# Kernel optimization log

Hardware: AMD Instinct MI355X
Metric: run time of the kernel (lower is better)

The kernel has to match this reference:

```python
import jax, jax.numpy as jnp
import numpy as np

DC_WZ = 15
ETA = 0.1
RADIUS = DC_WZ // 2  # 7
EPS = 1e-3


def avg_pool2d(x, k, pad):
    # torch F.avg_pool2d default: zero padding, count_include_pad=True -> divide by k*k always
    s = jax.lax.reduce_window(
        x, 0.0, jax.lax.add,
        window_dimensions=(1, 1, k, k),
        window_strides=(1, 1, 1, 1),
        padding=[(0, 0), (0, 0), (pad, pad), (pad, pad)])
    return s / float(k * k)


def min_pool2d_replicate(x, k, pad):
    # replicate (edge) pad then VALID min-pool, matching -max_pool2d(-pad(x, replicate))
    xp = jnp.pad(x, ((0, 0), (0, 0), (pad, pad), (pad, pad)), mode='edge')
    return jax.lax.reduce_window(
        xp, jnp.inf, jax.lax.min,
        window_dimensions=(1, 1, k, k),
        window_strides=(1, 1, 1, 1),
        padding='VALID')


def guided_filter(guide, src, radius, eps=EPS):
    k = 2 * radius + 1
    mean_I = avg_pool2d(guide, k, radius)
    mean_p = avg_pool2d(src, k, radius)
    mean_Ip = avg_pool2d(guide * src, k, radius)
    cov_Ip = mean_Ip - mean_I * mean_p
    mean_II = avg_pool2d(guide * guide, k, radius)
    var_I = mean_II - mean_I * mean_I
    a = cov_Ip / (var_I + eps)
    b = mean_p - a * mean_I
    mean_a = avg_pool2d(a, k, radius)
    mean_b = avg_pool2d(b, k, radius)
    return mean_a * guide + mean_b


def setup_inputs() -> dict:
    key = jax.random.key(0)
    k1, k2 = jax.random.split(key)
    smoky_image = jax.random.uniform(k1, (16, 3, 512, 512), dtype=jnp.float32)
    rho_DNN = jax.random.uniform(k2, (16, 3, 512, 512), dtype=jnp.float32)
    return {"smoky_image": smoky_image, "rho_DNN": rho_DNN}


def reference(smoky_image, rho_DNN):
    # dark channel: per-pixel min over RGB, then 15x15 min-pool with replicate pad
    dc_pixel = jnp.min(smoky_image, axis=-3, keepdims=True)  # [B,1,H,W]
    dc_coarse = min_pool2d_replicate(dc_pixel, DC_WZ, RADIUS)
    guide_I = jnp.mean(smoky_image, axis=-3, keepdims=True)
    dc_refined = guided_filter(guide_I, dc_coarse, RADIUS, EPS)
    dc_refined = jax.lax.stop_gradient(dc_refined)  # torch: no_grad + detach
    dc_rho = (ETA + dc_refined) / (ETA + 1.0) * (1.0 - rho_DNN)
    return smoky_image - dc_rho
```

## Files before the change

kernel.cpp:

```cpp
#include <hip/hip_runtime.h>

#define BATCH 16
#define HH 512
#define WW 512
#define PLANE (HH*WW)

#define LDS_WAIT()   asm volatile("s_waitcnt lgkmcnt(0)" ::: "memory")
#define WAVE_FENCE() asm volatile("" ::: "memory")

#define T1 64
#define HALO 7
#define LW (T1 + 2*HALO)

__global__ __launch_bounds__(256) void k1_guide_minpool(
    const float* __restrict__ smoky, float* __restrict__ guide, float* __restrict__ p)
{
    __shared__ float dcp[LW*LW];
    __shared__ float vmn[T1*LW];
    int nwg = gridDim.x;
    int wg = (blockIdx.x & 7) * (nwg >> 3) + (blockIdx.x >> 3);
    int img  = wg >> 6;
    int tile = wg & 63;
    int y0 = (tile >> 3) * T1;
    int x0 = (tile & 7) * T1;
    int t = threadIdx.x;
    const float* s0 = smoky + (size_t)img * 3 * PLANE;
    float* gpl = guide + (size_t)img * PLANE;
    float* ppl = p     + (size_t)img * PLANE;

    for (int i = t; i < LW*LW; i += 256) {
        int ly = i / LW, lx = i - ly * LW;
        int iy = y0 - HALO + ly, ix = x0 - HALO + lx;
        int cy = min(max(iy, 0), HH-1);
        int cx = min(max(ix, 0), WW-1);
        const float* bp = s0 + cy * WW + cx;
        float c0 = bp[0], c1 = bp[PLANE], c2 = bp[2*PLANE];
        dcp[i] = fminf(fminf(c0, c1), c2);
        if (ly >= HALO && ly < HALO+T1 && lx >= HALO && lx < HALO+T1)
            gpl[iy * WW + ix] = (c0 + c1 + c2) * (1.0f/3.0f);
    }
    __syncthreads();
    for (int i = t; i < T1*LW; i += 256) {
        int r = i / LW, c = i - r * LW;
        float m = dcp[r*LW + c];
        #pragma unroll
        for (int d = 1; d < 15; ++d) m = fminf(m, dcp[(r+d)*LW + c]);
        vmn[i] = m;
    }
    __syncthreads();
    for (int i = t; i < T1*T1; i += 256) {
        int r = i >> 6, c = i & 63;
        float m = vmn[r*LW + c];
        #pragma unroll
        for (int d = 1; d < 15; ++d) m = fminf(m, vmn[r*LW + c + d]);
        ppl[(y0+r)*WW + x0 + c] = m;
    }
}

#define RS2 16

__global__ __launch_bounds__(256) void k2_ab(
    const float* __restrict__ guide, const float* __restrict__ p,
    float* __restrict__ aO, float* __restrict__ bO)
{
    __shared__ float ls[4][4][80];
    int nwg = gridDim.x;
    int wg = (blockIdx.x & 7) * (nwg >> 3) + (blockIdx.x >> 3);
    int w = threadIdx.x >> 6, l = threadIdx.x & 63;
    int gw = wg * 4 + w;
    int img   = gw >> 8;
    int cg    = (gw >> 5) & 7;
    int strip = gw & 31;
    int y0 = strip * RS2;
    int c0 = cg * 64;
    const float* gP = guide + (size_t)img * PLANE;
    const float* pP = p     + (size_t)img * PLANE;
    float* aPl = aO + (size_t)img * PLANE;
    float* bPl = bO + (size_t)img * PLANE;

    int col0 = c0 - 7 + l;
    int col1 = c0 + 57 + l;
    bool v0 = (col0 >= 0);
    bool v1 = (l < 14) && (col1 < WW);

    float sI0=0,sII0=0,sP0=0,sIp0=0;
    float sI1=0,sII1=0,sP1=0,sIp1=0;

    auto loadrow = [&](int y, float& I0, float& Q0, float& I1, float& Q1) {
        I0 = 0.f; Q0 = 0.f; I1 = 0.f; Q1 = 0.f;
        if ((unsigned)y < (unsigned)HH) {
            const float* gr = gP + (size_t)y * WW;
            const float* pr = pP + (size_t)y * WW;
            if (v0) { I0 = gr[col0]; Q0 = pr[col0]; }
            if (v1) { I1 = gr[col1]; Q1 = pr[col1]; }
        }
    };

    for (int r = y0 - 8; r <= y0 + 6; ++r) {
        float I0,Q0,I1,Q1; loadrow(r, I0,Q0,I1,Q1);
        sI0+=I0; sII0+=I0*I0; sP0+=Q0; sIp0+=I0*Q0;
        sI1+=I1; sII1+=I1*I1; sP1+=Q1; sIp1+=I1*Q1;
    }
    float aI0,aQ0,aI1,aQ1, bI0,bQ0,bI1,bQ1;
    loadrow(y0 + 7, aI0,aQ0,aI1,aQ1);
    loadrow(y0 - 8, bI0,bQ0,bI1,bQ1);

    float* L = &ls[w][0][0];
    const float inv225 = 1.0f/225.0f;
    for (int y = y0; y < y0 + RS2; ++y) {
        sI0 += aI0 - bI0;  sII0 += aI0*aI0 - bI0*bI0;
        sP0 += aQ0 - bQ0;  sIp0 += aI0*aQ0 - bI0*bQ0;
        sI1 += aI1 - bI1;  sII1 += aI1*aI1 - bI1*bI1;
        sP1 += aQ1 - bQ1;  sIp1 += aI1*aQ1 - bI1*bQ1;
        loadrow(y + 8, aI0,aQ0,aI1,aQ1);
        loadrow(y - 7, bI0,bQ0,bI1,bQ1);
        L[l] = sI0; L[80+l] = sII0; L[160+l] = sP0; L[240+l] = sIp0;
        if (l < 14) { L[64+l] = sI1; L[144+l] = sII1; L[224+l] = sP1; L[304+l] = sIp1; }
        LDS_WAIT();
        float SI=0,SII=0,SP=0,SIp=0;
        #pragma unroll
        for (int d = 0; d < 15; ++d) {
            SI  += L[l+d];
            SII += L[80+l+d];
            SP  += L[160+l+d];
            SIp += L[240+l+d];
        }
        WAVE_FENCE();
        float mI = SI*inv225, mP = SP*inv225;
        float va = (SIp*inv225 - mI*mP) / (SII*inv225 - mI*mI + 1e-3f);
        size_t off = (size_t)y*WW + c0 + l;
        aPl[off] = va;
        bPl[off] = mP - va*mI;
    }
}

__global__ __launch_bounds__(256) void k3_final(
    const float* __restrict__ aI, const float* __restrict__ bI,
    const float* __restrict__ guide, const float* __restrict__ smoky,
    const float* __restrict__ rho, float* __restrict__ out)
{
    __shared__ float ls[4][2][80];
    int nwg = gridDim.x;
    int wg = (blockIdx.x & 7) * (nwg >> 3) + (blockIdx.x >> 3);
    int w = threadIdx.x >> 6, l = threadIdx.x & 63;
    int gw = wg * 4 + w;
    int img   = gw >> 8;
    int cg    = (gw >> 5) & 7;
    int strip = gw & 31;
    int y0 = strip * RS2;
    int c0 = cg * 64;
    const float* aP = aI + (size_t)img * PLANE;
    const float* bP = bI + (size_t)img * PLANE;
    const float* gP = guide + (size_t)img * PLANE;
    const float* sP = smoky + (size_t)img * 3 * PLANE;
    const float* rP = rho   + (size_t)img * 3 * PLANE;
    float* oP = out + (size_t)img * 3 * PLANE;

    int col0 = c0 - 7 + l;
    int col1 = c0 + 57 + l;
    bool v0 = (col0 >= 0);
    bool v1 = (l < 14) && (col1 < WW);

    float sa0=0, sb0=0, sa1=0, sb1=0;

    auto loadrow = [&](int y, float& A0, float& B0, float& A1, float& B1) {
        A0 = 0.f; B0 = 0.f; A1 = 0.f; B1 = 0.f;
        if ((unsigned)y < (unsigned)HH) {
            const float* ar = aP + (size_t)y * WW;
            const float* br = bP + (size_t)y * WW;
            if (v0) { A0 = ar[col0]; B0 = br[col0]; }
            if (v1) { A1 = ar[col1]; B1 = br[col1]; }
        }
    };

    for (int r = y0 - 8; r <= y0 + 6; ++r) {
        float A0,B0,A1,B1; loadrow(r, A0,B0,A1,B1);
        sa0+=A0; sb0+=B0; sa1+=A1; sb1+=B1;
    }
    float aa0,ab0,aa1,ab1, ba0,bb0,ba1,bb1;
    loadrow(y0 + 7, aa0,ab0,aa1,ab1);
    loadrow(y0 - 8, ba0,bb0,ba1,bb1);

    float eg, es0,es1,es2, er0,er1,er2;
    int yend = y0 + RS2;
    auto loademit = [&](int y) {
        if (y < yend) {
            size_t off = (size_t)y*WW + c0 + l;
            eg  = gP[off];
            es0 = sP[off]; es1 = sP[off+PLANE]; es2 = sP[off+2*PLANE];
            er0 = rP[off]; er1 = rP[off+PLANE]; er2 = rP[off+2*PLANE];
        }
    };
    loademit(y0);

    float* L = &ls[w][0][0];
    const float inv225 = 1.0f/225.0f;
    const float inv11  = 1.0f/1.1f;
    for (int y = y0; y < yend; ++y) {
        sa0 += aa0 - ba0;  sb0 += ab0 - bb0;
        sa1 += aa1 - ba1;  sb1 += ab1 - bb1;
        float g = eg, s0 = es0, s1 = es1, s2 = es2, r0 = er0, r1 = er1, r2 = er2;
        loadrow(y + 8, aa0,ab0,aa1,ab1);
        loadrow(y - 7, ba0,bb0,ba1,bb1);
        loademit(y + 1);
        L[l] = sa0; L[80+l] = sb0;
        if (l < 14) { L[64+l] = sa1; L[144+l] = sb1; }
        LDS_WAIT();
        float SA=0, SB=0;
        #pragma unroll
        for (int d = 0; d < 15; ++d) { SA += L[l+d]; SB += L[80+l+d]; }
        WAVE_FENCE();
        float dcr = SA*inv225*g + SB*inv225;
        float f = (0.1f + dcr) * inv11;
        size_t off = (size_t)y*WW + c0 + l;
        oP[off]          = s0 - f*(1.0f - r0);
        oP[off+PLANE]    = s1 - f*(1.0f - r1);
        oP[off+2*PLANE]  = s2 - f*(1.0f - r2);
    }
}

extern "C" void kernel_launch(void* const* d_in, const int* in_sizes, int n_in,
                              void* d_out, int out_size, void* d_ws, size_t ws_size,
                              hipStream_t stream) {
    const float* smoky = (const float*)d_in[0];
    const float* rho   = (const float*)d_in[1];
    float* out = (float*)d_out;
    float* ws  = (float*)d_ws;
    const size_t P = (size_t)BATCH * PLANE;
    float* guide = ws;
    float* p     = ws + P;
    float* a     = ws + 2*P;
    float* b     = ws + 3*P;

    k1_guide_minpool<<<BATCH*64, 256, 0, stream>>>(smoky, guide, p);
    k2_ab<<<BATCH*64, 256, 0, stream>>>(guide, p, a, b);
    k3_final<<<BATCH*64, 256, 0, stream>>>(a, b, guide, smoky, rho, out);
}
```

Baseline: 94.08 us.

## Halve row strips, interleave a/b into float2, double-buffer row loads

Cuts the row strip height from 16 to 8 and doubles the grid for the box-filter kernels, giving more waves to hide latency. The a and b coefficients are stored interleaved as one float2 array, so the final kernel reads one 8-byte value per pixel instead of two separate 4-byte loads. The sliding-window loops are unrolled by two with double-buffered prefetch of the add and subtract rows. The cost is more halo re-reading per strip (15 prologue rows for only 8 output rows) and higher register pressure.

```diff
diff --git a/kernel.cpp b/kernel.cpp
--- a/kernel.cpp
+++ b/kernel.cpp
@@ -57,26 +57,25 @@
     }
 }
 
-#define RS2 16
+#define RS2 8
 
 __global__ __launch_bounds__(256) void k2_ab(
     const float* __restrict__ guide, const float* __restrict__ p,
-    float* __restrict__ aO, float* __restrict__ bO)
+    float2* __restrict__ abO)
 {
     __shared__ float ls[4][4][80];
     int nwg = gridDim.x;
     int wg = (blockIdx.x & 7) * (nwg >> 3) + (blockIdx.x >> 3);
     int w = threadIdx.x >> 6, l = threadIdx.x & 63;
     int gw = wg * 4 + w;
-    int img   = gw >> 8;
-    int cg    = (gw >> 5) & 7;
-    int strip = gw & 31;
+    int img   = gw >> 9;
+    int cg    = (gw >> 6) & 7;
+    int strip = gw & 63;
     int y0 = strip * RS2;
     int c0 = cg * 64;
     const float* gP = guide + (size_t)img * PLANE;
     const float* pP = p     + (size_t)img * PLANE;
-    float* aPl = aO + (size_t)img * PLANE;
-    float* bPl = bO + (size_t)img * PLANE;
+    float2* abP = abO + (size_t)img * PLANE;
 
     int col0 = c0 - 7 + l;
     int col1 = c0 + 57 + l;
@@ -101,19 +100,11 @@
         sI0+=I0; sII0+=I0*I0; sP0+=Q0; sIp0+=I0*Q0;
         sI1+=I1; sII1+=I1*I1; sP1+=Q1; sIp1+=I1*Q1;
     }
-    float aI0,aQ0,aI1,aQ1, bI0,bQ0,bI1,bQ1;
-    loadrow(y0 + 7, aI0,aQ0,aI1,aQ1);
-    loadrow(y0 - 8, bI0,bQ0,bI1,bQ1);
 
     float* L = &ls[w][0][0];
     const float inv225 = 1.0f/225.0f;
-    for (int y = y0; y < y0 + RS2; ++y) {
-        sI0 += aI0 - bI0;  sII0 += aI0*aI0 - bI0*bI0;
-        sP0 += aQ0 - bQ0;  sIp0 += aI0*aQ0 - bI0*bQ0;
-        sI1 += aI1 - bI1;  sII1 += aI1*aI1 - bI1*bI1;
-        sP1 += aQ1 - bQ1;  sIp1 += aI1*aQ1 - bI1*bQ1;
-        loadrow(y + 8, aI0,aQ0,aI1,aQ1);
-        loadrow(y - 7, bI0,bQ0,bI1,bQ1);
+
+    auto emit = [&](int y) {
         L[l] = sI0; L[80+l] = sII0; L[160+l] = sP0; L[240+l] = sIp0;
         if (l < 14) { L[64+l] = sI1; L[144+l] = sII1; L[224+l] = sP1; L[304+l] = sIp1; }
         LDS_WAIT();
@@ -128,29 +119,50 @@
         WAVE_FENCE();
         float mI = SI*inv225, mP = SP*inv225;
         float va = (SIp*inv225 - mI*mP) / (SII*inv225 - mI*mI + 1e-3f);
-        size_t off = (size_t)y*WW + c0 + l;
-        aPl[off] = va;
-        bPl[off] = mP - va*mI;
+        abP[(size_t)y*WW + c0 + l] = make_float2(va, mP - va*mI);
+    };
+
+    float aI0A,aQ0A,aI1A,aQ1A, bI0A,bQ0A,bI1A,bQ1A;
+    float aI0B,aQ0B,aI1B,aQ1B, bI0B,bQ0B,bI1B,bQ1B;
+    loadrow(y0 + 7, aI0A,aQ0A,aI1A,aQ1A);
+    loadrow(y0 - 8, bI0A,bQ0A,bI1A,bQ1A);
+    loadrow(y0 + 8, aI0B,aQ0B,aI1B,aQ1B);
+    loadrow(y0 - 7, bI0B,bQ0B,bI1B,bQ1B);
+
+    for (int y = y0; y < y0 + RS2; y += 2) {
+        sI0 += aI0A - bI0A;  sII0 += aI0A*aI0A - bI0A*bI0A;
+        sP0 += aQ0A - bQ0A;  sIp0 += aI0A*aQ0A - bI0A*bQ0A;
+        sI1 += aI1A - bI1A;  sII1 += aI1A*aI1A - bI1A*bI1A;
+        sP1 += aQ1A - bQ1A;  sIp1 += aI1A*aQ1A - bI1A*bQ1A;
+        loadrow(y + 9, aI0A,aQ0A,aI1A,aQ1A);
+        loadrow(y - 6, bI0A,bQ0A,bI1A,bQ1A);
+        emit(y);
+        sI0 += aI0B - bI0B;  sII0 += aI0B*aI0B - bI0B*bI0B;
+        sP0 += aQ0B - bQ0B;  sIp0 += aI0B*aQ0B - bI0B*bQ0B;
+        sI1 += aI1B - bI1B;  sII1 += aI1B*aI1B - bI1B*bI1B;
+        sP1 += aQ1B - bQ1B;  sIp1 += aI1B*aQ1B - bI1B*bQ1B;
+        loadrow(y + 10, aI0B,aQ0B,aI1B,aQ1B);
+        loadrow(y - 5,  bI0B,bQ0B,bI1B,bQ1B);
+        emit(y + 1);
     }
 }
 
 __global__ __launch_bounds__(256) void k3_final(
-    const float* __restrict__ aI, const float* __restrict__ bI,
-    const float* __restrict__ guide, const float* __restrict__ smoky,
-    const float* __restrict__ rho, float* __restrict__ out)
+    const float2* __restrict__ abI, const float* __restrict__ guide,
+    const float* __restrict__ smoky, const float* __restrict__ rho,
+    float* __restrict__ out)
 {
     __shared__ float ls[4][2][80];
     int nwg = gridDim.x;
     int wg = (blockIdx.x & 7) * (nwg >> 3) + (blockIdx.x >> 3);
     int w = threadIdx.x >> 6, l = threadIdx.x & 63;
     int gw = wg * 4 + w;
-    int img   = gw >> 8;
-    int cg    = (gw >> 5) & 7;
-    int strip = gw & 31;
+    int img   = gw >> 9;
+    int cg    = (gw >> 6) & 7;
+    int strip = gw & 63;
     int y0 = strip * RS2;
     int c0 = cg * 64;
-    const float* aP = aI + (size_t)img * PLANE;
-    const float* bP = bI + (size_t)img * PLANE;
+    const float2* abP = abI + (size_t)img * PLANE;
     const float* gP = guide + (size_t)img * PLANE;
     const float* sP = smoky + (size_t)img * 3 * PLANE;
     const float* rP = rho   + (size_t)img * 3 * PLANE;
@@ -163,27 +175,23 @@
 
     float sa0=0, sb0=0, sa1=0, sb1=0;
 
-    auto loadrow = [&](int y, float& A0, float& B0, float& A1, float& B1) {
-        A0 = 0.f; B0 = 0.f; A1 = 0.f; B1 = 0.f;
+    auto loadrow = [&](int y, float2& P0, float2& P1) {
+        P0 = make_float2(0.f, 0.f); P1 = make_float2(0.f, 0.f);
         if ((unsigned)y < (unsigned)HH) {
-            const float* ar = aP + (size_t)y * WW;
-            const float* br = bP + (size_t)y * WW;
-            if (v0) { A0 = ar[col0]; B0 = br[col0]; }
-            if (v1) { A1 = ar[col1]; B1 = br[col1]; }
+            const float2* r = abP + (size_t)y * WW;
+            if (v0) P0 = r[col0];
+            if (v1) P1 = r[col1];
         }
     };
 
     for (int r = y0 - 8; r <= y0 + 6; ++r) {
-        float A0,B0,A1,B1; loadrow(r, A0,B0,A1,B1);
-        sa0+=A0; sb0+=B0; sa1+=A1; sb1+=B1;
-    }
-    float aa0,ab0,aa1,ab1, ba0,bb0,ba1,bb1;
-    loadrow(y0 + 7, aa0,ab0,aa1,ab1);
-    loadrow(y0 - 8, ba0,bb0,ba1,bb1);
-
-    float eg, es0,es1,es2, er0,er1,er2;
+        float2 P0, P1; loadrow(r, P0, P1);
+        sa0 += P0.x; sb0 += P0.y; sa1 += P1.x; sb1 += P1.y;
+    }
+
     int yend = y0 + RS2;
-    auto loademit = [&](int y) {
+    auto loademit = [&](int y, float& eg, float& es0, float& es1, float& es2,
+                        float& er0, float& er1, float& er2) {
         if (y < yend) {
             size_t off = (size_t)y*WW + c0 + l;
             eg  = gP[off];
@@ -191,18 +199,13 @@
             er0 = rP[off]; er1 = rP[off+PLANE]; er2 = rP[off+2*PLANE];
         }
     };
-    loademit(y0);
 
     float* L = &ls[w][0][0];
     const float inv225 = 1.0f/225.0f;
     const float inv11  = 1.0f/1.1f;
-    for (int y = y0; y < yend; ++y) {
-        sa0 += aa0 - ba0;  sb0 += ab0 - bb0;
-        sa1 += aa1 - ba1;  sb1 += ab1 - bb1;
-        float g = eg, s0 = es0, s1 = es1, s2 = es2, r0 = er0, r1 = er1, r2 = er2;
-        loadrow(y + 8, aa0,ab0,aa1,ab1);
-        loadrow(y - 7, ba0,bb0,ba1,bb1);
-        loademit(y + 1);
+
+    auto emit = [&](int y, float g, float s0, float s1, float s2,
+                    float r0, float r1, float r2) {
         L[l] = sa0; L[80+l] = sb0;
         if (l < 14) { L[64+l] = sa1; L[144+l] = sb1; }
         LDS_WAIT();
@@ -216,6 +219,36 @@
         oP[off]          = s0 - f*(1.0f - r0);
         oP[off+PLANE]    = s1 - f*(1.0f - r1);
         oP[off+2*PLANE]  = s2 - f*(1.0f - r2);
+    };
+
+    float2 addA0, addA1, subA0, subA1;
+    float2 addB0, addB1, subB0, subB1;
+    float egA,esA0,esA1,esA2,erA0,erA1,erA2;
+    float egB,esB0,esB1,esB2,erB0,erB1,erB2;
+    loadrow(y0 + 7, addA0, addA1);
+    loadrow(y0 - 8, subA0, subA1);
+    loademit(y0, egA,esA0,esA1,esA2,erA0,erA1,erA2);
+    loadrow(y0 + 8, addB0, addB1);
+    loadrow(y0 - 7, subB0, subB1);
+    loademit(y0 + 1, egB,esB0,esB1,esB2,erB0,erB1,erB2);
+
+    for (int y = y0; y < yend; y += 2) {
+        sa0 += addA0.x - subA0.x;  sb0 += addA0.y - subA0.y;
+        sa1 += addA1.x - subA1.x;  sb1 += addA1.y - subA1.y;
+        float g = egA, s0 = esA0, s1 = esA1, s2 = esA2;
+        float r0 = erA0, r1 = erA1, r2 = erA2;
+        loadrow(y + 9, addA0, addA1);
+        loadrow(y - 6, subA0, subA1);
+        loademit(y + 2, egA,esA0,esA1,esA2,erA0,erA1,erA2);
+        emit(y, g, s0, s1, s2, r0, r1, r2);
+        sa0 += addB0.x - subB0.x;  sb0 += addB0.y - subB0.y;
+        sa1 += addB1.x - subB1.x;  sb1 += addB1.y - subB1.y;
+        g = egB; s0 = esB0; s1 = esB1; s2 = esB2;
+        r0 = erB0; r1 = erB1; r2 = erB2;
+        loadrow(y + 10, addB0, addB1);
+        loadrow(y - 5,  subB0, subB1);
+        loademit(y + 3, egB,esB0,esB1,esB2,erB0,erB1,erB2);
+        emit(y + 1, g, s0, s1, s2, r0, r1, r2);
     }
 }
 
@@ -229,10 +262,9 @@
     const size_t P = (size_t)BATCH * PLANE;
     float* guide = ws;
     float* p     = ws + P;
-    float* a     = ws + 2*P;
-    float* b     = ws + 3*P;
+    float2* ab   = (float2*)(ws + 2*P);
 
     k1_guide_minpool<<<BATCH*64, 256, 0, stream>>>(smoky, guide, p);
-    k2_ab<<<BATCH*64, 256, 0, stream>>>(guide, p, a, b);
-    k3_final<<<BATCH*64, 256, 0, stream>>>(a, b, guide, smoky, rho, out);
-}
+    k2_ab<<<BATCH*128, 256, 0, stream>>>(guide, p, ab);
+    k3_final<<<BATCH*128, 256, 0, stream>>>(ab, guide, smoky, rho, out);
+}
```

Result: slower. 98.58 us (+4.8%).
